# Kernel tuning notes

Hardware: AMD Instinct MI355X
Metric: run time of the kernel (lower is better)

The kernel has to match this reference:

```python
import jax, jax.numpy as jnp
import numpy as np

D_MODEL = 1024
N_HEADS = 16
ALPHA = 0.7
C_PARAM = 5
CUTOFF = C_PARAM // 2 + 1  # 3
LN_EPS = 1e-12
B, S = 4, 2048


def setup_inputs() -> dict:
    key = jax.random.key(0)
    ks = jax.random.split(key, 10)
    d = D_MODEL
    scale = 1.0 / np.sqrt(d)
    return {
        "input_tensor": jax.random.normal(ks[0], (B, S, d), dtype=jnp.float32),
        "attention_mask": jnp.ones((1, 1, S, S), dtype=jnp.int32),
        "sqrt_beta": jax.random.normal(ks[1], (1, 1, d), dtype=jnp.float32),
        "ln_gamma": jnp.ones((d,), dtype=jnp.float32),
        "ln_beta": jnp.zeros((d,), dtype=jnp.float32),
        "q_w": jax.random.normal(ks[2], (d, d), dtype=jnp.float32) * scale,
        "q_b": jnp.zeros((d,), dtype=jnp.float32),
        "k_w": jax.random.normal(ks[3], (d, d), dtype=jnp.float32) * scale,
        "k_b": jnp.zeros((d,), dtype=jnp.float32),
        "v_w": jax.random.normal(ks[4], (d, d), dtype=jnp.float32) * scale,
        "v_b": jnp.zeros((d,), dtype=jnp.float32),
    }


def _layer_norm(x, g, b):
    mu = jnp.mean(x, axis=-1, keepdims=True)
    var = jnp.mean(jnp.square(x - mu), axis=-1, keepdims=True)
    return (x - mu) * jax.lax.rsqrt(var + LN_EPS) * g + b


def bsarec_layer(x, mask, sqrt_beta, ln_gamma, ln_beta, q_w, q_b, k_w, k_b, v_w, v_b):
    batch, seq_len, hidden = x.shape
    # ---- FrequencyLayer (DSP branch) ----
    xf = jnp.fft.rfft(x, axis=1, norm='ortho')                 # [B, S//2+1, D]
    freq = jnp.arange(xf.shape[1])[None, :, None]
    low_pass = jnp.fft.irfft(jnp.where(freq < CUTOFF, xf, 0.0), n=seq_len, axis=1, norm='ortho')
    high_pass = x - low_pass
    seq_fft = low_pass + jnp.square(sqrt_beta) * high_pass
    dsp = _layer_norm(seq_fft + x, ln_gamma, ln_beta)          # dropout=0 -> identity
    # ---- MultiHeadAttention (GSP branch) ----
    h, d_k = N_HEADS, hidden // N_HEADS
    def split(t):  # [B,S,D] -> [B,H,S,d_k]
        return t.reshape(batch, seq_len, h, d_k).transpose(0, 2, 1, 3)
    q = split(x @ q_w.T + q_b)
    k = split(x @ k_w.T + k_b)
    v = split(x @ v_w.T + v_b)
    scores = jnp.einsum('bhsd,bhtd->bhst', q, k) / jnp.sqrt(jnp.float32(d_k))
    scores = jnp.where(mask == 0, -jnp.inf, scores)
    scores = scores - jnp.max(scores)                           # global max, as in source
    p = jax.nn.softmax(scores, axis=-1)
    p = jnp.where(jnp.isnan(p), 0.0, p)
    out = jnp.einsum('bhst,bhtd->bhsd', p, v)
    gsp = out.transpose(0, 2, 1, 3).reshape(batch, seq_len, hidden)
    return ALPHA * dsp + (1.0 - ALPHA) * gsp


def reference(input_tensor, attention_mask, sqrt_beta, ln_gamma, ln_beta, q_w, q_b, k_w, k_b, v_w, v_b):
    return bsarec_layer(input_tensor, attention_mask, sqrt_beta, ln_gamma, ln_beta,
                        q_w, q_b, k_w, k_b, v_w, v_b)
```

## Files before the change

kernel.cpp:

```cpp
#include <hip/hip_runtime.h>

#define S_LEN 2048
#define DM 1024
#define NB 4
#define NROWS (NB * S_LEN)
#define NHEADS 16
#define DK 64

typedef __bf16 bf16x8 __attribute__((ext_vector_type(8)));
typedef __bf16 bf16x2 __attribute__((ext_vector_type(2)));
typedef float f32x4 __attribute__((ext_vector_type(4)));
typedef float f32x2 __attribute__((ext_vector_type(2)));
typedef unsigned u32x4 __attribute__((ext_vector_type(4)));

struct __align__(8) us4 { unsigned short x, y, z, w; };

__device__ __forceinline__ unsigned cvt2(float a, float b) {
    f32x2 t; t.x = a; t.y = b;
    bf16x2 h = __builtin_convertvector(t, bf16x2);
    return __builtin_bit_cast(unsigned, h);
}
__device__ __forceinline__ unsigned short f2bf(float f) {
    __bf16 h = (__bf16)f;
    return __builtin_bit_cast(unsigned short, h);
}

__device__ __forceinline__ void gl2lds16(const void* g, void* l) {
    __builtin_amdgcn_global_load_lds(
        (const __attribute__((address_space(1))) unsigned int*)g,
        (__attribute__((address_space(3))) unsigned int*)l, 16, 0, 0);
}

#if __has_builtin(__builtin_amdgcn_exp2f)
#define EXP2F(x) __builtin_amdgcn_exp2f(x)
#else
#define EXP2F(x) exp2f(x)
#endif

__global__ __launch_bounds__(256) void prep(
    const float* __restrict__ x, float* __restrict__ coef,
    unsigned short* __restrict__ xbf, const float* __restrict__ qw,
    const float* __restrict__ kw, const float* __restrict__ vw,
    unsigned short* __restrict__ wbf) {
    int bx = blockIdx.x;
    int tid = threadIdx.x;
    if (bx >= 256) {
        int widx = ((bx - 256) * 256 + tid) * 4;
        int which = widx >> 20, off = widx & 0xFFFFF;
        const float* src = (which == 0) ? qw : ((which == 1) ? kw : vw);
        float4 v = *(const float4*)(&src[off]);
        uint2 pk; pk.x = cvt2(v.x, v.y); pk.y = cvt2(v.z, v.w);
        *(uint2*)(&wbf[widx]) = pk;
        return;
    }
    int b = bx >> 6, tc = bx & 63;
    int d0 = tid * 4;
    __shared__ float tw[4][32];
    if (tid < 32) {
        const float omega = 6.283185307179586476925f / (float)S_LEN;
        float sn, cs;
        __sincosf(omega * (float)(tc * 32 + tid), &sn, &cs);
        tw[0][tid] = sn;
        tw[1][tid] = cs;
        tw[2][tid] = 2.f * sn * cs;
        tw[3][tid] = cs * cs - sn * sn;
    }
    __syncthreads();
    float4 a0 = {0, 0, 0, 0}, a1 = {0, 0, 0, 0}, b1 = {0, 0, 0, 0},
           a2 = {0, 0, 0, 0}, b2 = {0, 0, 0, 0};
    for (int i = 0; i < 32; ++i) {
        int t = tc * 32 + i;
        long idx = (long)(b * S_LEN + t) * DM + d0;
        float4 v = *(const float4*)(&x[idx]);
        uint2 pk; pk.x = cvt2(v.x, v.y); pk.y = cvt2(v.z, v.w);
        *(uint2*)(&xbf[idx]) = pk;
        float sn = tw[0][i], cs = tw[1][i], s2 = tw[2][i], c2 = tw[3][i];
#pragma unroll
        for (int j = 0; j < 4; ++j) {
            float vv = (&v.x)[j];
            (&a0.x)[j] += vv;
            (&a1.x)[j] += vv * cs;
            (&b1.x)[j] += vv * sn;
            (&a2.x)[j] += vv * c2;
            (&b2.x)[j] += vv * s2;
        }
    }
    int base = b * DM + d0;
#pragma unroll
    for (int j = 0; j < 4; ++j) {
        atomicAdd(&coef[0 * 4096 + base + j], (&a0.x)[j]);
        atomicAdd(&coef[1 * 4096 + base + j], (&a1.x)[j]);
        atomicAdd(&coef[2 * 4096 + base + j], (&b1.x)[j]);
        atomicAdd(&coef[3 * 4096 + base + j], (&a2.x)[j]);
        atomicAdd(&coef[4 * 4096 + base + j], (&b2.x)[j]);
    }
}

__global__ __launch_bounds__(256) void dsp_ln(
    const float* __restrict__ x, const float* __restrict__ coef,
    const float* __restrict__ sqrt_beta, const float* __restrict__ gamma,
    const float* __restrict__ beta, const unsigned short* __restrict__ Og,
    float* __restrict__ out) {
    int row = blockIdx.x;
    int b = row >> 11, t = row & (S_LEN - 1);
    int tid = threadIdx.x, lane = tid & 63, wave = tid >> 6;
    const float omega = 6.283185307179586476925f / (float)S_LEN;
    float sn, cs;
    __sincosf(omega * (float)t, &sn, &cs);
    float c2t = cs * cs - sn * sn, s2t = 2.f * sn * cs;
    int d0 = tid * 4;
    long base = (long)row * DM;
    float4 xv = *(const float4*)(&x[base + d0]);
    int cb = b * DM + d0;
    float4 C0 = *(const float4*)(&coef[0 * 4096 + cb]);
    float4 C1 = *(const float4*)(&coef[1 * 4096 + cb]);
    float4 S1 = *(const float4*)(&coef[2 * 4096 + cb]);
    float4 C2 = *(const float4*)(&coef[3 * 4096 + cb]);
    float4 S2 = *(const float4*)(&coef[4 * 4096 + cb]);
    float4 sb = *(const float4*)(&sqrt_beta[d0]);
    const float inv_s = 1.0f / (float)S_LEN;
    float y[4];
#pragma unroll
    for (int i = 0; i < 4; ++i) {
        float c0 = (&C0.x)[i], c1 = (&C1.x)[i], s1 = (&S1.x)[i],
              c2 = (&C2.x)[i], s2 = (&S2.x)[i];
        float lp = (c0 + 2.f * (c1 * cs + s1 * sn) + 2.f * (c2 * c2t + s2 * s2t)) * inv_s;
        float xx = (&xv.x)[i];
        float b2 = (&sb.x)[i];
        b2 = b2 * b2;
        y[i] = xx + lp + b2 * (xx - lp);
    }
    float ssum = y[0] + y[1] + y[2] + y[3];
    float ssq = y[0] * y[0] + y[1] * y[1] + y[2] * y[2] + y[3] * y[3];
#pragma unroll
    for (int m = 1; m < 64; m <<= 1) {
        ssum += __shfl_xor(ssum, m, 64);
        ssq += __shfl_xor(ssq, m, 64);
    }
    __shared__ float red[8];
    if (lane == 0) { red[wave] = ssum; red[4 + wave] = ssq; }
    __syncthreads();
    float S = red[0] + red[1] + red[2] + red[3];
    float SQ = red[4] + red[5] + red[6] + red[7];
    float mu = S * (1.0f / DM);
    float var = SQ * (1.0f / DM) - mu * mu;
    float rstd = rsqrtf(var + 1e-12f);
    float4 g = *(const float4*)(&gamma[d0]);
    float4 be = *(const float4*)(&beta[d0]);
    us4 gv = *(const us4*)(&Og[((long)((b << 4) + (d0 >> 6)) * S_LEN + t) * DK + (d0 & 63)]);
    const unsigned short* gp = (const unsigned short*)&gv;
    float4 o;
#pragma unroll
    for (int i = 0; i < 4; ++i)
        (&o.x)[i] = 0.7f * ((y[i] - mu) * rstd * (&g.x)[i] + (&be.x)[i]) +
                    0.3f * __uint_as_float((unsigned)gp[i] << 16);
    *(float4*)(&out[base + d0]) = o;
}

__global__ __launch_bounds__(512, 2) void gemm_qkv(
    const unsigned short* __restrict__ A, const unsigned short* __restrict__ W,
    const float* __restrict__ qb, const float* __restrict__ kb,
    const float* __restrict__ vb, unsigned short* __restrict__ Qo,
    unsigned short* __restrict__ Ko, unsigned short* __restrict__ Vt_g) {
    const int m0 = blockIdx.y * 256;
    const int n0g = blockIdx.x * 256;
    const int which = n0g >> 10;
    const int n0 = n0g & 1023;
    const int tid = threadIdx.x;
    const int lane = tid & 63, wave = tid >> 6;
    const int wm = wave >> 2, wn = wave & 3;
    const int r = lane & 15, q = lane >> 4;
    __shared__ __align__(16) unsigned short SmF[4 * 16384];
    const int scol = ((lane & 3) ^ ((lane >> 3) & 3)) * 8;
    const int rs = (q ^ ((r >> 1) & 3)) * 8;
    f32x4 acc[8][4] = {};

#define GST(slot_, kt_)                                                     \
    do {                                                                    \
        const int ko_ = (kt_) * 32;                                         \
        _Pragma("unroll")                                                   \
        for (int e = 0; e < 2; ++e) {                                       \
            int cA = e * 8 + wave;                                          \
            int grow = cA * 16 + (lane >> 2);                               \
            gl2lds16(&A[(long)(m0 + grow) * DM + ko_ + scol],               \
                     &SmF[(slot_) * 16384 + cA * 512 + lane * 8]);          \
            gl2lds16(&W[(long)(n0g + grow) * DM + ko_ + scol],              \
                     &SmF[(slot_) * 16384 + 8192 + cA * 512 + lane * 8]);   \
        }                                                                   \
    } while (0)

    GST(0, 0);
    GST(1, 1);
    asm volatile("s_waitcnt vmcnt(4)" ::: "memory");
    __builtin_amdgcn_s_barrier();

    for (int kti = 0; kti < 32; ++kti) {
        const int slot = kti & 3;
        if (kti < 30) GST((kti + 2) & 3, kti + 2);
        const unsigned short* Ac = &SmF[slot * 16384];
        const unsigned short* Bc = Ac + 8192;
        bf16x8 bfr[4];
#pragma unroll
        for (int ni = 0; ni < 4; ++ni)
            bfr[ni] = *(const bf16x8*)(&Bc[(wn * 64 + ni * 16 + r) * 32 + rs]);
        __builtin_amdgcn_s_setprio(1);
#pragma unroll
        for (int mh = 0; mh < 2; ++mh) {
            bf16x8 af[4];
#pragma unroll
            for (int i = 0; i < 4; ++i)
                af[i] = *(const bf16x8*)(
                    &Ac[(wm * 128 + (mh * 4 + i) * 16 + r) * 32 + rs]);
#pragma unroll
            for (int i = 0; i < 4; ++i)
#pragma unroll
                for (int ni = 0; ni < 4; ++ni)
                    acc[mh * 4 + i][ni] = __builtin_amdgcn_mfma_f32_16x16x32_bf16(
                        af[i], bfr[ni], acc[mh * 4 + i][ni], 0, 0, 0);
        }
        __builtin_amdgcn_s_setprio(0);
        if (kti < 31) {
            if (kti < 30) {
                asm volatile("s_waitcnt vmcnt(4)" ::: "memory");
            } else {
                asm volatile("s_waitcnt vmcnt(0)" ::: "memory");
            }
            __builtin_amdgcn_s_barrier();
        }
    }
#undef GST
    __syncthreads();

    const float* bias = (which == 0) ? qb : ((which == 1) ? kb : vb);
    if (which < 2) {
        const float qs = (which == 0) ? 0.18033688011112042f : 1.0f;
        unsigned short* Out = (which == 0) ? Qo : Ko;
#pragma unroll
        for (int strip = 0; strip < 2; ++strip) {
            if (strip) __syncthreads();
            if (wm == strip) {
#pragma unroll
                for (int mi = 0; mi < 8; ++mi) {
                    int row = mi * 16 + q * 4;
#pragma unroll
                    for (int ni = 0; ni < 4; ++ni) {
                        int col = wn * 64 + ni * 16 + r;
                        float bv = bias[n0 + col];
#pragma unroll
                        for (int reg = 0; reg < 4; ++reg)
                            SmF[(row + reg) * 264 + col] =
                                f2bf((acc[mi][ni][reg] + bv) * qs);
                    }
                }
            }
            __syncthreads();
#pragma unroll
            for (int p = 0; p < 8; ++p) {
                int row = p * 16 + wave * 2 + (lane >> 5);
                int cc = (lane & 31) * 8;
                uint4 v = *(const uint4*)(&SmF[row * 264 + cc]);
                long gb = (long)(m0 + strip * 128 + row) * DM + n0 + cc;
                *(uint4*)(&Out[gb]) = v;
            }
        }
    } else {
        const int bb = m0 >> 11, sg = m0 & (S_LEN - 1);
#pragma unroll
        for (int strip = 0; strip < 2; ++strip) {
            if (strip) __syncthreads();
            if (wm == strip) {
#pragma unroll
                for (int ni = 0; ni < 4; ++ni) {
                    int col = wn * 64 + ni * 16 + r;
                    float bv = bias[n0 + col];
#pragma unroll
                    for (int mi = 0; mi < 8; ++mi) {
                        int row = mi * 16 + q * 4;
                        *(unsigned*)(&SmF[col * 136 + row]) =
                            cvt2(acc[mi][ni][0] + bv, acc[mi][ni][1] + bv);
                        *(unsigned*)(&SmF[col * 136 + row + 2]) =
                            cvt2(acc[mi][ni][2] + bv, acc[mi][ni][3] + bv);
                    }
                }
            }
            __syncthreads();
#pragma unroll
            for (int p = 0; p < 8; ++p) {
                int n = p * 32 + wave * 4 + (lane >> 4);
                int mcc = (lane & 15) * 8;
                uint4 v = *(const uint4*)(&SmF[n * 136 + mcc]);
                long gb = ((long)bb * DM + n0 + n) * S_LEN + sg + strip * 128 + mcc;
                *(uint4*)(&Vt_g[gb]) = v;
            }
        }
    }
}

__global__ __launch_bounds__(128, 2) void attn(
    const unsigned short* __restrict__ Q, const unsigned short* __restrict__ K,
    const unsigned short* __restrict__ Vt_g, unsigned short* __restrict__ Og) {
    int bx = blockIdx.x;
    int bh = bx & 63, qt = bx >> 6;
    int b = bh >> 4, h = bh & 15;
    const int tid = threadIdx.x, lane = tid & 63, wave = tid >> 6;
    const int r = lane & 15, q = lane >> 4;
    const int hc = h * DK;
    const int q0 = qt * 128 + wave * 64;

    bf16x8 aq[4][2];
#pragma unroll
    for (int mt = 0; mt < 4; ++mt) {
        long rowQ = (long)(b * S_LEN + q0 + mt * 16 + r) * DM + hc;
        aq[mt][0] = *(const bf16x8*)(&Q[rowQ + q * 8]);
        aq[mt][1] = *(const bf16x8*)(&Q[rowQ + 32 + q * 8]);
    }

    __shared__ __align__(16) unsigned short Ks[2][4096];
    __shared__ __align__(16) unsigned short Vt[2][4096];
    __shared__ float denL[128];

    f32x4 accO[4][4] = {};
    float den[4] = {};

    const int lr = lane >> 3, lc = lane & 7;
    const unsigned short* kp[4];
    const unsigned short* vp[4];
    int ld[4];
#pragma unroll
    for (int e = 0; e < 4; ++e) {
        int cw = wave * 4 + e;
        int row = cw * 8 + lr;
        int cg = lc ^ lr ^ ((e & 1) << 2);
        ld[e] = cw * 512;
        kp[e] = K + (long)(b * S_LEN + row) * DM + hc + cg * 8;
        vp[e] = Vt_g + (long)(bh * 64 + row) * S_LEN + cg * 8;
    }

    const int lo = r & 3, hi = r >> 2;
    const int abase = (hi * 8 + lo) * 64;
    const int ca = (q ^ lo ^ ((hi & 1) << 2)) * 8;
    const int cb2 = ca ^ 32;
    const int va0 = (q ^ (r & 7) ^ (((r >> 3) & 1) << 2)) * 8;
    const int va1 = va0 ^ 32;

#define STAGE(buf)                                            \
    do {                                                      \
        _Pragma("unroll")                                     \
        for (int e = 0; e < 4; ++e) {                         \
            gl2lds16(kp[e], &Ks[buf][ld[e] + lane * 8]);      \
            gl2lds16(vp[e], &Vt[buf][ld[e] + lane * 8]);      \
            kp[e] += 64 * DM; vp[e] += 64;                    \
        }                                                     \
    } while (0)

    STAGE(0);
    asm volatile("s_waitcnt vmcnt(0)" ::: "memory");
    __builtin_amdgcn_s_barrier();

    for (int t = 0; t < 32; ++t) {
        const int cur = t & 1;
        if (t < 31) STAGE(cur ^ 1);
        const unsigned short* Kc = Ks[cur];
        const unsigned short* Vc = Vt[cur];
        __builtin_amdgcn_s_setprio(1);
#pragma unroll
        for (int c = 0; c < 2; ++c) {
            const int cb64 = c * 2048;
            bf16x8 ak00 = *(const bf16x8*)(&Kc[cb64 + abase + ca]);
            bf16x8 ak01 = *(const bf16x8*)(&Kc[cb64 + abase + cb2]);
            bf16x8 ak10 = *(const bf16x8*)(&Kc[cb64 + 256 + abase + cb2]);
            bf16x8 ak11 = *(const bf16x8*)(&Kc[cb64 + 256 + abase + ca]);
            const int va = c ? va1 : va0;
            bf16x8 bv[4];
            bv[0] = *(const bf16x8*)(&Vc[(0 * 16 + r) * 64 + va]);
            bv[1] = *(const bf16x8*)(&Vc[(1 * 16 + r) * 64 + va]);
            bv[2] = *(const bf16x8*)(&Vc[(2 * 16 + r) * 64 + va]);
            bv[3] = *(const bf16x8*)(&Vc[(3 * 16 + r) * 64 + va]);
#pragma unroll
            for (int mt = 0; mt < 4; ++mt) {
                f32x4 sa = {}, sb = {};
                sa = __builtin_amdgcn_mfma_f32_16x16x32_bf16(ak00, aq[mt][0], sa, 0, 0, 0);
                sa = __builtin_amdgcn_mfma_f32_16x16x32_bf16(ak01, aq[mt][1], sa, 0, 0, 0);
                sb = __builtin_amdgcn_mfma_f32_16x16x32_bf16(ak10, aq[mt][0], sb, 0, 0, 0);
                sb = __builtin_amdgcn_mfma_f32_16x16x32_bf16(ak11, aq[mt][1], sb, 0, 0, 0);
                float p0 = EXP2F(sa[0]), p1 = EXP2F(sa[1]);
                float p2 = EXP2F(sa[2]), p3 = EXP2F(sa[3]);
                float p4 = EXP2F(sb[0]), p5 = EXP2F(sb[1]);
                float p6 = EXP2F(sb[2]), p7 = EXP2F(sb[3]);
                den[mt] += ((p0 + p1) + (p2 + p3)) + ((p4 + p5) + (p6 + p7));
                u32x4 wv;
                wv.x = cvt2(p0, p1); wv.y = cvt2(p2, p3);
                wv.z = cvt2(p4, p5); wv.w = cvt2(p6, p7);
                bf16x8 ap = __builtin_bit_cast(bf16x8, wv);
#pragma unroll
                for (int dt = 0; dt < 4; ++dt)
                    accO[mt][dt] = __builtin_amdgcn_mfma_f32_16x16x32_bf16(
                        ap, bv[dt], accO[mt][dt], 0, 0, 0);
            }
        }
        __builtin_amdgcn_s_setprio(0);
        asm volatile("s_waitcnt vmcnt(0)" ::: "memory");
        __builtin_amdgcn_s_barrier();
    }
#undef STAGE

#pragma unroll
    for (int mt = 0; mt < 4; ++mt) {
        float d = den[mt];
        d += __shfl_xor(d, 16, 64);
        d += __shfl_xor(d, 32, 64);
        if (q == 0) denL[wave * 64 + mt * 16 + r] = d;
    }
#pragma unroll
    for (int mt = 0; mt < 4; ++mt) {
        float4 dv = *(const float4*)(&denL[wave * 64 + mt * 16 + q * 4]);
        float rs[4];
#pragma unroll
        for (int reg = 0; reg < 4; ++reg) rs[reg] = 1.0f / (&dv.x)[reg];
        long obase = (long)bh * S_LEN + q0 + mt * 16 + q * 4;
#pragma unroll
        for (int dt = 0; dt < 4; ++dt) {
            int col = dt * 16 + r;
#pragma unroll
            for (int reg = 0; reg < 4; ++reg)
                Og[(obase + reg) * DK + col] = f2bf(accO[mt][dt][reg] * rs[reg]);
        }
    }
}

extern "C" void kernel_launch(void* const* d_in, const int* in_sizes, int n_in,
                              void* d_out, int out_size, void* d_ws, size_t ws_size,
                              hipStream_t stream) {
    const float* x = (const float*)d_in[0];
    const float* sqrt_beta = (const float*)d_in[2];
    const float* gamma = (const float*)d_in[3];
    const float* beta = (const float*)d_in[4];
    const float* qw = (const float*)d_in[5];
    const float* qb = (const float*)d_in[6];
    const float* kw = (const float*)d_in[7];
    const float* kb = (const float*)d_in[8];
    const float* vw = (const float*)d_in[9];
    const float* vb = (const float*)d_in[10];
    float* out = (float*)d_out;

    char* ws = (char*)d_ws;
    float* coef = (float*)ws;
    unsigned short* xbf = (unsigned short*)(ws + 81920);
    unsigned short* wbf = (unsigned short*)(ws + 81920 + 16777216);
    unsigned short* Qb = (unsigned short*)(ws + 81920 + 16777216 + 6291456);
    unsigned short* Kb = Qb + (long)NROWS * DM;
    unsigned short* Vt_g = Kb + (long)NROWS * DM;
    unsigned short* Og = xbf;

    hipMemsetAsync(coef, 0, 5 * 4096 * sizeof(float), stream);
    prep<<<3328, 256, 0, stream>>>(x, coef, xbf, qw, kw, vw, wbf);
    dim3 ggrid(3 * DM / 256, NROWS / 256);
    gemm_qkv<<<ggrid, 512, 0, stream>>>(xbf, wbf, qb, kb, vb, Qb, Kb, Vt_g);
    attn<<<NB * NHEADS * (S_LEN / 128), 128, 0, stream>>>(Qb, Kb, Vt_g, Og);
    dsp_ln<<<NROWS, 256, 0, stream>>>(x, coef, sqrt_beta, gamma, beta, Og, out);
}
```

Baseline: 284.1 us.

## Split GEMM k-step into two phased halves and double attention block query tile

The QKV GEMM main loop now runs each k-step as two half-phases. Each phase loads half of the A fragments, issues half of the next-tile global-to-LDS copies, and synchronizes with explicit barriers and sched_barrier fences, so memory traffic interleaves with MFMA work. The attention kernel now uses 4 waves (256 query rows) per block instead of 2, so each staged K/V tile is shared by twice as many queries and every thread issues fewer loads. The cost is extra barriers per GEMM iteration and fewer, larger attention blocks, which may hurt occupancy or tail balance.

```diff
diff --git a/kernel.cpp b/kernel.cpp
--- a/kernel.cpp
+++ b/kernel.cpp
@@ -175,60 +175,71 @@
     const int rs = (q ^ ((r >> 1) & 3)) * 8;
     f32x4 acc[8][4] = {};
 
-#define GST(slot_, kt_)                                                     \
+#define GSTH(slot_, kt_, e_)                                                \
     do {                                                                    \
         const int ko_ = (kt_) * 32;                                         \
-        _Pragma("unroll")                                                   \
-        for (int e = 0; e < 2; ++e) {                                       \
-            int cA = e * 8 + wave;                                          \
-            int grow = cA * 16 + (lane >> 2);                               \
-            gl2lds16(&A[(long)(m0 + grow) * DM + ko_ + scol],               \
-                     &SmF[(slot_) * 16384 + cA * 512 + lane * 8]);          \
-            gl2lds16(&W[(long)(n0g + grow) * DM + ko_ + scol],              \
-                     &SmF[(slot_) * 16384 + 8192 + cA * 512 + lane * 8]);   \
-        }                                                                   \
+        int cA = (e_) * 8 + wave;                                           \
+        int grow = cA * 16 + (lane >> 2);                                   \
+        gl2lds16(&A[(long)(m0 + grow) * DM + ko_ + scol],                   \
+                 &SmF[(slot_) * 16384 + cA * 512 + lane * 8]);              \
+        gl2lds16(&W[(long)(n0g + grow) * DM + ko_ + scol],                  \
+                 &SmF[(slot_) * 16384 + 8192 + cA * 512 + lane * 8]);       \
     } while (0)
 
-    GST(0, 0);
-    GST(1, 1);
+    GSTH(0, 0, 0); GSTH(0, 0, 1);
+    GSTH(1, 1, 0); GSTH(1, 1, 1);
     asm volatile("s_waitcnt vmcnt(4)" ::: "memory");
     __builtin_amdgcn_s_barrier();
 
     for (int kti = 0; kti < 32; ++kti) {
         const int slot = kti & 3;
-        if (kti < 30) GST((kti + 2) & 3, kti + 2);
         const unsigned short* Ac = &SmF[slot * 16384];
         const unsigned short* Bc = Ac + 8192;
-        bf16x8 bfr[4];
+        bf16x8 bfr[4], af[4];
 #pragma unroll
         for (int ni = 0; ni < 4; ++ni)
             bfr[ni] = *(const bf16x8*)(&Bc[(wn * 64 + ni * 16 + r) * 32 + rs]);
+#pragma unroll
+        for (int i = 0; i < 4; ++i)
+            af[i] = *(const bf16x8*)(&Ac[(wm * 128 + i * 16 + r) * 32 + rs]);
+        if (kti < 30) GSTH((kti + 2) & 3, kti + 2, 0);
+        __builtin_amdgcn_sched_barrier(0);
+        __builtin_amdgcn_s_barrier();
+        asm volatile("s_waitcnt lgkmcnt(0)" ::: "memory");
+        __builtin_amdgcn_sched_barrier(0);
         __builtin_amdgcn_s_setprio(1);
 #pragma unroll
-        for (int mh = 0; mh < 2; ++mh) {
-            bf16x8 af[4];
-#pragma unroll
-            for (int i = 0; i < 4; ++i)
-                af[i] = *(const bf16x8*)(
-                    &Ac[(wm * 128 + (mh * 4 + i) * 16 + r) * 32 + rs]);
-#pragma unroll
-            for (int i = 0; i < 4; ++i)
-#pragma unroll
-                for (int ni = 0; ni < 4; ++ni)
-                    acc[mh * 4 + i][ni] = __builtin_amdgcn_mfma_f32_16x16x32_bf16(
-                        af[i], bfr[ni], acc[mh * 4 + i][ni], 0, 0, 0);
-        }
+        for (int i = 0; i < 4; ++i)
+#pragma unroll
+            for (int ni = 0; ni < 4; ++ni)
+                acc[i][ni] = __builtin_amdgcn_mfma_f32_16x16x32_bf16(
+                    af[i], bfr[ni], acc[i][ni], 0, 0, 0);
         __builtin_amdgcn_s_setprio(0);
-        if (kti < 31) {
-            if (kti < 30) {
-                asm volatile("s_waitcnt vmcnt(4)" ::: "memory");
-            } else {
-                asm volatile("s_waitcnt vmcnt(0)" ::: "memory");
-            }
-            __builtin_amdgcn_s_barrier();
-        }
-    }
-#undef GST
+        __builtin_amdgcn_s_barrier();
+#pragma unroll
+        for (int i = 0; i < 4; ++i)
+            af[i] = *(const bf16x8*)(&Ac[(wm * 128 + (4 + i) * 16 + r) * 32 + rs]);
+        if (kti < 30) GSTH((kti + 2) & 3, kti + 2, 1);
+        __builtin_amdgcn_sched_barrier(0);
+        __builtin_amdgcn_s_barrier();
+        asm volatile("s_waitcnt lgkmcnt(0)" ::: "memory");
+        __builtin_amdgcn_sched_barrier(0);
+        __builtin_amdgcn_s_setprio(1);
+#pragma unroll
+        for (int i = 0; i < 4; ++i)
+#pragma unroll
+            for (int ni = 0; ni < 4; ++ni)
+                acc[4 + i][ni] = __builtin_amdgcn_mfma_f32_16x16x32_bf16(
+                    af[i], bfr[ni], acc[4 + i][ni], 0, 0, 0);
+        __builtin_amdgcn_s_setprio(0);
+        if (kti < 30) {
+            asm volatile("s_waitcnt vmcnt(4)" ::: "memory");
+        } else if (kti == 30) {
+            asm volatile("s_waitcnt vmcnt(0)" ::: "memory");
+        }
+        __builtin_amdgcn_s_barrier();
+    }
+#undef GSTH
     __syncthreads();
 
     const float* bias = (which == 0) ? qb : ((which == 1) ? kb : vb);
@@ -296,7 +307,7 @@
     }
 }
 
-__global__ __launch_bounds__(128, 2) void attn(
+__global__ __launch_bounds__(256, 2) void attn(
     const unsigned short* __restrict__ Q, const unsigned short* __restrict__ K,
     const unsigned short* __restrict__ Vt_g, unsigned short* __restrict__ Og) {
     int bx = blockIdx.x;
@@ -305,7 +316,7 @@
     const int tid = threadIdx.x, lane = tid & 63, wave = tid >> 6;
     const int r = lane & 15, q = lane >> 4;
     const int hc = h * DK;
-    const int q0 = qt * 128 + wave * 64;
+    const int q0 = qt * 256 + wave * 64;
 
     bf16x8 aq[4][2];
 #pragma unroll
@@ -317,24 +328,21 @@
 
     __shared__ __align__(16) unsigned short Ks[2][4096];
     __shared__ __align__(16) unsigned short Vt[2][4096];
-    __shared__ float denL[128];
+    __shared__ float denL[256];
 
     f32x4 accO[4][4] = {};
     float den[4] = {};
 
     const int lr = lane >> 3, lc = lane & 7;
-    const unsigned short* kp[4];
-    const unsigned short* vp[4];
-    int ld[4];
-#pragma unroll
-    for (int e = 0; e < 4; ++e) {
-        int cw = wave * 4 + e;
-        int row = cw * 8 + lr;
-        int cg = lc ^ lr ^ ((e & 1) << 2);
-        ld[e] = cw * 512;
-        kp[e] = K + (long)(b * S_LEN + row) * DM + hc + cg * 8;
-        vp[e] = Vt_g + (long)(bh * 64 + row) * S_LEN + cg * 8;
-    }
+    const int cw0 = wave * 2, cw1 = cw0 + 1;
+    const int ld0 = cw0 * 512, ld1 = cw1 * 512;
+    const int row0 = cw0 * 8 + lr, row1 = cw1 * 8 + lr;
+    const int cg0 = lc ^ lr;
+    const int cg1 = lc ^ lr ^ 4;
+    const unsigned short* kp0 = K + (long)(b * S_LEN + row0) * DM + hc + cg0 * 8;
+    const unsigned short* kp1 = K + (long)(b * S_LEN + row1) * DM + hc + cg1 * 8;
+    const unsigned short* vp0 = Vt_g + (long)(bh * 64 + row0) * S_LEN + cg0 * 8;
+    const unsigned short* vp1 = Vt_g + (long)(bh * 64 + row1) * S_LEN + cg1 * 8;
 
     const int lo = r & 3, hi = r >> 2;
     const int abase = (hi * 8 + lo) * 64;
@@ -343,14 +351,13 @@
     const int va0 = (q ^ (r & 7) ^ (((r >> 3) & 1) << 2)) * 8;
     const int va1 = va0 ^ 32;
 
-#define STAGE(buf)                                            \
-    do {                                                      \
-        _Pragma("unroll")                                     \
-        for (int e = 0; e < 4; ++e) {                         \
-            gl2lds16(kp[e], &Ks[buf][ld[e] + lane * 8]);      \
-            gl2lds16(vp[e], &Vt[buf][ld[e] + lane * 8]);      \
-            kp[e] += 64 * DM; vp[e] += 64;                    \
-        }                                                     \
+#define STAGE(buf)                                    \
+    do {                                              \
+        gl2lds16(kp0, &Ks[buf][ld0 + lane * 8]);      \
+        gl2lds16(kp1, &Ks[buf][ld1 + lane * 8]);      \
+        gl2lds16(vp0, &Vt[buf][ld0 + lane * 8]);      \
+        gl2lds16(vp1, &Vt[buf][ld1 + lane * 8]);      \
+        kp0 += 64 * DM; kp1 += 64 * DM; vp0 += 64; vp1 += 64; \
     } while (0)
 
     STAGE(0);
@@ -456,6 +463,6 @@
     prep<<<3328, 256, 0, stream>>>(x, coef, xbf, qw, kw, vw, wbf);
     dim3 ggrid(3 * DM / 256, NROWS / 256);
     gemm_qkv<<<ggrid, 512, 0, stream>>>(xbf, wbf, qb, kb, vb, Qb, Kb, Vt_g);
-    attn<<<NB * NHEADS * (S_LEN / 128), 128, 0, stream>>>(Qb, Kb, Vt_g, Og);
+    attn<<<NB * NHEADS * (S_LEN / 256), 256, 0, stream>>>(Qb, Kb, Vt_g, Og);
     dsp_ln<<<NROWS, 256, 0, stream>>>(x, coef, sqrt_beta, gamma, beta, Og, out);
 }
```

New measurement: 285.5 us. About the same (+0.5%).
